# Kernel tuning notes

Measured on AMD Instinct MI355X. Metric: run time of the kernel, lower is better.

The kernel has to match this reference:

```python
import jax, jax.numpy as jnp
import numpy as np


def _make_phi() -> np.ndarray:
    """G2 associative 3-form phi on Im(O): fully antisymmetric 7x7x7.
    Convention (Bryant): phi = e123 + e145 + e167 + e246 - e257 - e347 - e356 (1-based).
    """
    triples = [
        (0, 1, 2, 1.0), (0, 3, 4, 1.0), (0, 5, 6, 1.0), (1, 3, 5, 1.0),
        (1, 4, 6, -1.0), (2, 3, 6, -1.0), (2, 4, 5, -1.0),
    ]
    phi = np.zeros((7, 7, 7), dtype=np.float32)
    for i, j, k, s in triples:
        # antisymmetrize: even permutations +s, odd permutations -s
        phi[i, j, k] = s; phi[j, k, i] = s; phi[k, i, j] = s
        phi[j, i, k] = -s; phi[i, k, j] = -s; phi[k, j, i] = -s
    return phi

_PHI = jnp.asarray(_make_phi())


def setup_inputs() -> dict:
    key = jax.random.key(0)
    kx, ky, kz = jax.random.split(key, 3)
    shape = (256, 16384, 7)
    return {
        "x": jax.random.normal(kx, shape, dtype=jnp.float32),
        "y": jax.random.normal(ky, shape, dtype=jnp.float32),
        "z": jax.random.normal(kz, shape, dtype=jnp.float32),
    }


def reference(x, y, z):
    phi = _PHI.astype(x.dtype)
    norm = lambda v: jnp.linalg.norm(v, axis=-1, keepdims=True)
    dot = lambda a, b: jnp.sum(a * b, axis=-1, keepdims=True)

    # cross product via phi: (x x y)_k = phi_ijk x_i y_j
    cross_xy = jnp.einsum('ijk,...i,...j->...k', phi, x, y)

    # triple products phi(a, b, c) = phi_ijk a_i b_j c_k
    triple = lambda a, b, c: jnp.einsum('ijk,...i,...j,...k->...', phi, a, b, c)[..., None]

    features = [
        norm(x),          # ||x||
        dot(x, y),        # <x, y>
        norm(y),          # ||y||
        norm(cross_xy),   # ||x x y||
        dot(x, z),        # <x, z>
        dot(y, z),        # <y, z>
        norm(z),          # ||z||
        triple(x, y, z),  # phi(x, y, z)
        triple(x, x, y),  # phi(x, x, y) (identically 0 by antisymmetry, kept for fidelity)
        triple(y, y, z),  # phi(y, y, z) (identically 0 by antisymmetry, kept for fidelity)
    ]
    return jnp.concatenate(features, axis=-1)  # [..., 10]
```

## Files before the change

kernel.cpp:

```cpp
#include <hip/hip_runtime.h>

#define NPB 256

__global__ __launch_bounds__(256) void g2_invariant_kernel(
        const float* __restrict__ x,
        const float* __restrict__ y,
        const float* __restrict__ z,
        float* __restrict__ out,
        int npts) {
    __shared__ float sx[NPB * 7];
    __shared__ float sy[NPB * 7];
    __shared__ float sz[NPB * 7];
    __shared__ float so[NPB * 10];

    const int t = threadIdx.x;
    const size_t p0 = (size_t)blockIdx.x * NPB;
    const int cnt = (int)min((long long)NPB, (long long)npts - (long long)p0);

    if (cnt == NPB) {
        const float4* gx = (const float4*)(x + p0 * 7);
        const float4* gy = (const float4*)(y + p0 * 7);
        const float4* gz = (const float4*)(z + p0 * 7);
        float4* lx = (float4*)sx;
        float4* ly = (float4*)sy;
        float4* lz = (float4*)sz;
        for (int i = t; i < NPB * 7 / 4; i += 256) {
            lx[i] = gx[i];
            ly[i] = gy[i];
            lz[i] = gz[i];
        }
    } else if (cnt > 0) {
        for (int i = t; i < cnt * 7; i += 256) {
            sx[i] = x[p0 * 7 + i];
            sy[i] = y[p0 * 7 + i];
            sz[i] = z[p0 * 7 + i];
        }
    }
    __syncthreads();

    if (t < cnt) {
        float X[7], Y[7], Z[7];
#pragma unroll
        for (int c = 0; c < 7; ++c) {
            X[c] = sx[t * 7 + c];
            Y[c] = sy[t * 7 + c];
            Z[c] = sz[t * 7 + c];
        }
        float sxx = 0.f, sxy = 0.f, syy = 0.f, sxz = 0.f, syz = 0.f, szz = 0.f;
#pragma unroll
        for (int c = 0; c < 7; ++c) {
            sxx = fmaf(X[c], X[c], sxx);
            sxy = fmaf(X[c], Y[c], sxy);
            syy = fmaf(Y[c], Y[c], syy);
            sxz = fmaf(X[c], Z[c], sxz);
            syz = fmaf(Y[c], Z[c], syz);
            szz = fmaf(Z[c], Z[c], szz);
        }
#define W(a, b) (X[a] * Y[b] - X[b] * Y[a])
        const float c0 = W(1, 2) + W(3, 4) + W(5, 6);
        const float c1 = W(2, 0) + W(3, 5) - W(4, 6);
        const float c2 = W(0, 1) - W(3, 6) - W(4, 5);
        const float c3 = W(4, 0) + W(5, 1) - W(6, 2);
        const float c4 = W(0, 3) + W(1, 6) + W(2, 5);
        const float c5 = W(6, 0) + W(1, 3) - W(2, 4);
        const float c6 = W(0, 5) - W(1, 4) - W(2, 3);
#undef W
        const float scc = c0 * c0 + c1 * c1 + c2 * c2 + c3 * c3 +
                          c4 * c4 + c5 * c5 + c6 * c6;
        const float tr = c0 * Z[0] + c1 * Z[1] + c2 * Z[2] + c3 * Z[3] +
                         c4 * Z[4] + c5 * Z[5] + c6 * Z[6];

        float* o = &so[t * 10];
        o[0] = sqrtf(sxx);
        o[1] = sxy;
        o[2] = sqrtf(syy);
        o[3] = sqrtf(scc);
        o[4] = sxz;
        o[5] = syz;
        o[6] = sqrtf(szz);
        o[7] = tr;
        o[8] = 0.f;
        o[9] = 0.f;
    }
    __syncthreads();

    if (cnt == NPB) {
        float4* go = (float4*)(out + p0 * 10);
        const float4* lo = (const float4*)so;
        for (int i = t; i < NPB * 10 / 4; i += 256) go[i] = lo[i];
    } else if (cnt > 0) {
        for (int i = t; i < cnt * 10; i += 256) out[p0 * 10 + i] = so[i];
    }
}

extern "C" void kernel_launch(void* const* d_in, const int* in_sizes, int n_in,
                              void* d_out, int out_size, void* d_ws, size_t ws_size,
                              hipStream_t stream) {
    const float* x = (const float*)d_in[0];
    const float* y = (const float*)d_in[1];
    const float* z = (const float*)d_in[2];
    float* out = (float*)d_out;
    const int npts = in_sizes[0] / 7;
    const int nblocks = (npts + NPB - 1) / NPB;
    g2_invariant_kernel<<<nblocks, 256, 0, stream>>>(x, y, z, out, npts);
}
```

Before: 99.84 us.

## Replace LDS staging with per-thread register tiles of four points

Each thread now loads four consecutive points directly from global memory as vector loads into registers, computes the invariants, and writes results with nontemporal vector stores. This removes the shared-memory staging and the two block barriers. In exchange, each wavefront's load instructions touch addresses strided by 112 bytes rather than contiguous ones, and register use per thread rises considerably.

```diff
diff --git a/kernel.cpp b/kernel.cpp
--- a/kernel.cpp
+++ b/kernel.cpp
@@ -1,95 +1,90 @@
 #include <hip/hip_runtime.h>
 
-#define NPB 256
 
-__global__ __launch_bounds__(256) void g2_invariant_kernel(
+typedef float floatx4 __attribute__((ext_vector_type(4)));
+
+__device__ __forceinline__ void g2_point(const float* __restrict__ X,
+                                         const float* __restrict__ Y,
+                                         const float* __restrict__ Z,
+                                         float* __restrict__ o) {
+    float sxx = 0.f, sxy = 0.f, syy = 0.f, sxz = 0.f, syz = 0.f, szz = 0.f;
+#pragma unroll
+    for (int c = 0; c < 7; ++c) {
+        sxx = fmaf(X[c], X[c], sxx);
+        sxy = fmaf(X[c], Y[c], sxy);
+        syy = fmaf(Y[c], Y[c], syy);
+        sxz = fmaf(X[c], Z[c], sxz);
+        syz = fmaf(Y[c], Z[c], syz);
+        szz = fmaf(Z[c], Z[c], szz);
+    }
+#define W(a, b) (X[a] * Y[b] - X[b] * Y[a])
+    const float c0 = W(1, 2) + W(3, 4) + W(5, 6);
+    const float c1 = W(2, 0) + W(3, 5) - W(4, 6);
+    const float c2 = W(0, 1) - W(3, 6) - W(4, 5);
+    const float c3 = W(4, 0) + W(5, 1) - W(6, 2);
+    const float c4 = W(0, 3) + W(1, 6) + W(2, 5);
+    const float c5 = W(6, 0) + W(1, 3) - W(2, 4);
+    const float c6 = W(0, 5) - W(1, 4) - W(2, 3);
+#undef W
+    const float scc = c0 * c0 + c1 * c1 + c2 * c2 + c3 * c3 +
+                      c4 * c4 + c5 * c5 + c6 * c6;
+    const float tr = c0 * Z[0] + c1 * Z[1] + c2 * Z[2] + c3 * Z[3] +
+                     c4 * Z[4] + c5 * Z[5] + c6 * Z[6];
+    o[0] = sqrtf(sxx);
+    o[1] = sxy;
+    o[2] = sqrtf(syy);
+    o[3] = sqrtf(scc);
+    o[4] = sxz;
+    o[5] = syz;
+    o[6] = sqrtf(szz);
+    o[7] = tr;
+    o[8] = 0.f;
+    o[9] = 0.f;
+}
+
+__global__ __launch_bounds__(256, 2) void g2_reg_kernel(
         const float* __restrict__ x,
         const float* __restrict__ y,
         const float* __restrict__ z,
         float* __restrict__ out,
         int npts) {
-    __shared__ float sx[NPB * 7];
-    __shared__ float sy[NPB * 7];
-    __shared__ float sz[NPB * 7];
-    __shared__ float so[NPB * 10];
+    const int g = blockIdx.x * 256 + threadIdx.x;
+    const long long pbase = (long long)g * 4;
+    if (pbase >= npts) return;
 
-    const int t = threadIdx.x;
-    const size_t p0 = (size_t)blockIdx.x * NPB;
-    const int cnt = (int)min((long long)NPB, (long long)npts - (long long)p0);
-
-    if (cnt == NPB) {
-        const float4* gx = (const float4*)(x + p0 * 7);
-        const float4* gy = (const float4*)(y + p0 * 7);
-        const float4* gz = (const float4*)(z + p0 * 7);
-        float4* lx = (float4*)sx;
-        float4* ly = (float4*)sy;
-        float4* lz = (float4*)sz;
-        for (int i = t; i < NPB * 7 / 4; i += 256) {
-            lx[i] = gx[i];
-            ly[i] = gy[i];
-            lz[i] = gz[i];
+    if (pbase + 4 <= npts) {
+        float ax[28], ay[28], az[28], o[40];
+        const floatx4* x4 = (const floatx4*)x + (size_t)g * 7;
+        const floatx4* y4 = (const floatx4*)y + (size_t)g * 7;
+        const floatx4* z4 = (const floatx4*)z + (size_t)g * 7;
+#pragma unroll
+        for (int i = 0; i < 7; ++i) {
+            *(floatx4*)&ax[4 * i] = x4[i];
+            *(floatx4*)&ay[4 * i] = y4[i];
+            *(floatx4*)&az[4 * i] = z4[i];
         }
-    } else if (cnt > 0) {
-        for (int i = t; i < cnt * 7; i += 256) {
-            sx[i] = x[p0 * 7 + i];
-            sy[i] = y[p0 * 7 + i];
-            sz[i] = z[p0 * 7 + i];
+#pragma unroll
+        for (int p = 0; p < 4; ++p) {
+            g2_point(&ax[7 * p], &ay[7 * p], &az[7 * p], &o[10 * p]);
         }
-    }
-    __syncthreads();
-
-    if (t < cnt) {
-        float X[7], Y[7], Z[7];
+        floatx4* o4 = (floatx4*)out + (size_t)g * 10;
 #pragma unroll
-        for (int c = 0; c < 7; ++c) {
-            X[c] = sx[t * 7 + c];
-            Y[c] = sy[t * 7 + c];
-            Z[c] = sz[t * 7 + c];
+        for (int i = 0; i < 10; ++i) {
+            __builtin_nontemporal_store(*(floatx4*)&o[4 * i], o4 + i);
         }
-        float sxx = 0.f, sxy = 0.f, syy = 0.f, sxz = 0.f, syz = 0.f, szz = 0.f;
+    } else {
+        for (long long p = pbase; p < npts; ++p) {
+            float X[7], Y[7], Z[7], o[10];
 #pragma unroll
-        for (int c = 0; c < 7; ++c) {
-            sxx = fmaf(X[c], X[c], sxx);
-            sxy = fmaf(X[c], Y[c], sxy);
-            syy = fmaf(Y[c], Y[c], syy);
-            sxz = fmaf(X[c], Z[c], sxz);
-            syz = fmaf(Y[c], Z[c], syz);
-            szz = fmaf(Z[c], Z[c], szz);
+            for (int c = 0; c < 7; ++c) {
+                X[c] = x[p * 7 + c];
+                Y[c] = y[p * 7 + c];
+                Z[c] = z[p * 7 + c];
+            }
+            g2_point(X, Y, Z, o);
+#pragma unroll
+            for (int k = 0; k < 10; ++k) out[p * 10 + k] = o[k];
         }
-#define W(a, b) (X[a] * Y[b] - X[b] * Y[a])
-        const float c0 = W(1, 2) + W(3, 4) + W(5, 6);
-        const float c1 = W(2, 0) + W(3, 5) - W(4, 6);
-        const float c2 = W(0, 1) - W(3, 6) - W(4, 5);
-        const float c3 = W(4, 0) + W(5, 1) - W(6, 2);
-        const float c4 = W(0, 3) + W(1, 6) + W(2, 5);
-        const float c5 = W(6, 0) + W(1, 3) - W(2, 4);
-        const float c6 = W(0, 5) - W(1, 4) - W(2, 3);
-#undef W
-        const float scc = c0 * c0 + c1 * c1 + c2 * c2 + c3 * c3 +
-                          c4 * c4 + c5 * c5 + c6 * c6;
-        const float tr = c0 * Z[0] + c1 * Z[1] + c2 * Z[2] + c3 * Z[3] +
-                         c4 * Z[4] + c5 * Z[5] + c6 * Z[6];
-
-        float* o = &so[t * 10];
-        o[0] = sqrtf(sxx);
-        o[1] = sxy;
-        o[2] = sqrtf(syy);
-        o[3] = sqrtf(scc);
-        o[4] = sxz;
-        o[5] = syz;
-        o[6] = sqrtf(szz);
-        o[7] = tr;
-        o[8] = 0.f;
-        o[9] = 0.f;
-    }
-    __syncthreads();
-
-    if (cnt == NPB) {
-        float4* go = (float4*)(out + p0 * 10);
-        const float4* lo = (const float4*)so;
-        for (int i = t; i < NPB * 10 / 4; i += 256) go[i] = lo[i];
-    } else if (cnt > 0) {
-        for (int i = t; i < cnt * 10; i += 256) out[p0 * 10 + i] = so[i];
     }
 }
 
@@ -101,6 +96,7 @@
     const float* z = (const float*)d_in[2];
     float* out = (float*)d_out;
     const int npts = in_sizes[0] / 7;
-    const int nblocks = (npts + NPB - 1) / NPB;
-    g2_invariant_kernel<<<nblocks, 256, 0, stream>>>(x, y, z, out, npts);
+    const int ngroups = (npts + 3) / 4;
+    const int nblocks = (ngroups + 255) / 256;
+    g2_reg_kernel<<<nblocks, 256, 0, stream>>>(x, y, z, out, npts);
 }
```

New measurement: 352.6 us. +253.2%, slower.
